# Kernel optimization log

Hardware: AMD Instinct MI355X
Metric: run time of the kernel (lower is better)

The kernel has to match this reference:

```python
import jax, jax.numpy as jnp
import numpy as np

N = 2048          # nodes
IN_DIM = 512      # in_dim
H = 8             # num_heads
HD = IN_DIM // H  # head_dim = 64
L = 5             # max_path_len
E = 32768         # edges
D_EDGE = 64       # edge_feat_dim


def setup_inputs() -> dict:
    key = jax.random.key(0)
    ks = jax.random.split(key, 14)
    w = 1.0 / np.sqrt(IN_DIM)
    return {
        "node_feat": jax.random.normal(ks[0], (N, IN_DIM), jnp.float32),
        "edge_index": jax.random.randint(ks[1], (2, E), 0, N, dtype=jnp.int32),
        "max_path_len": 5,
        "shortest_distances": jax.random.randint(ks[2], (N, N), 0, L + 1, dtype=jnp.int32),
        "shortest_paths": jax.random.randint(ks[3], (N, N, L), 0, E + 1, dtype=jnp.int32),  # E == padding row
        "edge_feat": jax.random.normal(ks[4], (E, D_EDGE), jnp.float32),
        "attention_mask": jnp.zeros((N, N), jnp.int32),
        "WQ": jax.random.normal(ks[5], (IN_DIM, IN_DIM), jnp.float32) * w,
        "bQ": jax.random.normal(ks[6], (IN_DIM,), jnp.float32) * 0.02,
        "WK": jax.random.normal(ks[7], (IN_DIM, IN_DIM), jnp.float32) * w,
        "bK": jax.random.normal(ks[8], (IN_DIM,), jnp.float32) * 0.02,
        "WV": jax.random.normal(ks[9], (IN_DIM, IN_DIM), jnp.float32) * w,
        "bV": jax.random.normal(ks[10], (IN_DIM,), jnp.float32) * 0.02,
        "WO": jax.random.normal(ks[11], (IN_DIM, IN_DIM), jnp.float32) * w,
        "bO": jnp.zeros((IN_DIM,), jnp.float32),
        "spatial_bias": jax.random.normal(ks[12], ((L + 1) * H, 1), jnp.float32) * 0.02,
        "edge_weight": jax.random.normal(ks[13], ((L + 1) * H, D_EDGE), jnp.float32) * 0.02,
    }


def reference(node_feat, edge_index, max_path_len, shortest_distances, shortest_paths,
              edge_feat, attention_mask, WQ, bQ, WK, bK, WV, bV, WO, bO,
              spatial_bias, edge_weight):
    Nn, D = node_feat.shape
    Lp = max_path_len  # min(max_path_len, max_shortest_path_len); distances reach Lp here

    Q = (node_feat @ WQ + bQ).reshape(Nn, H, HD)
    K = (node_feat @ WK + bK).reshape(Nn, H, HD)
    V = (node_feat @ WV + bV).reshape(Nn, H, HD)

    # QK^T / sqrt(head_dim), laid out [N, N, H] as in the original after permute
    scores = jnp.einsum('nhd,mhd->nmh', Q, K) / np.sqrt(HD).astype(np.float32)

    # SpatialEncoding: bias table [(L+1)*H, 1] -> [L+1, H]; gather by clamped distance
    sp_table = spatial_bias.reshape(Lp + 1, H)
    dist = jnp.clip(shortest_distances, 0, Lp)
    scores = scores + sp_table[dist]  # [N, N, H]

    # EdgeEncoding: einsum('xyld,ldh->xyh') refactored as per-edge projection then gather
    W_e = edge_weight[: Lp * H].reshape(Lp, H, D_EDGE)  # (reshape[L,H,D].permute -> [L,D,H])
    padded = jnp.concatenate([edge_feat, jnp.zeros((1, D_EDGE), edge_feat.dtype)], axis=0)
    T = jnp.einsum('ed,lhd->elh', padded, W_e)  # [E+1, L, H]
    sp = shortest_paths[:, :, :Lp]
    gathered = T[sp, jnp.arange(Lp)[None, None, :]]  # [N, N, L, H]
    scores = scores + gathered.sum(axis=2)

    mask = attention_mask.astype(bool)
    scores = jnp.where(mask[:, :, None], -jnp.inf, scores)

    # NOTE: original applies softmax over dim=-1 of the [N, N, H] tensor (the head axis);
    # faithfully reproduced here. Dropout is identity (eval / p for inference).
    attn = jax.nn.softmax(scores, axis=-1)

    out = jnp.einsum('nmh,mhd->nhd', attn, V).reshape(Nn, D)
    return out @ WO + bO
```

## Files before the change

kernel.cpp:

```cpp
#include <hip/hip_runtime.h>

#define NN     2048
#define DIM    512
#define NH     8
#define HD     64
#define NE     32768
#define EPAD   32832
#define CHUNKS 4
#define LOG2E  1.4426950408889634f

typedef __attribute__((ext_vector_type(8))) short bf16x8;
typedef __attribute__((ext_vector_type(4))) float f32x4;

#define MFMA(a,b,c) __builtin_amdgcn_mfma_f32_16x16x32_bf16((a),(b),(c),0,0,0)

__device__ __forceinline__ float bf2f(unsigned int u16){
  union { unsigned int i; float f; } v; v.i = u16 << 16; return v.f;
}
__device__ __forceinline__ unsigned short f2bf(float f){
  union { float ff; unsigned int i; } v; v.ff = f;
  return (unsigned short)((v.i + 0x7fffu + ((v.i >> 16) & 1u)) >> 16);
}

__global__ __launch_bounds__(256) void cvt_k(
    const float* __restrict__ X, const float* __restrict__ ef, const float* __restrict__ ew,
    unsigned short* __restrict__ Xb, unsigned short* __restrict__ pEF, unsigned short* __restrict__ pEW)
{
  long g = (long)blockIdx.x*256 + threadIdx.x;
  const long GX = (long)NN*DIM/8;
  const long GE = (long)EPAD*8;
  const float* src; unsigned short* dst; long off, lim8;
  if (g < GX){ src = X;  dst = Xb;  off = g;        lim8 = GX; }
  else if (g < GX+GE){ src = ef; dst = pEF; off = g-GX; lim8 = (long)NE*8; }
  else { off = g-GX-GE; if (off >= 512) return; src = ew; dst = pEW; lim8 = 320; }
  unsigned short o[8];
  if (off < lim8){
    #pragma unroll
    for (int i=0;i<8;i++) o[i] = f2bf(src[off*8+i]);
  } else {
    #pragma unroll
    for (int i=0;i<8;i++) o[i] = 0;
  }
  *(uint4*)(dst + off*8) = *(const uint4*)o;
}

__global__ __launch_bounds__(256) void transpose512(
    const float* __restrict__ a0, const float* __restrict__ a1,
    const float* __restrict__ a2, const float* __restrict__ a3,
    unsigned short* __restrict__ out)
{
  __shared__ unsigned short tile[32][33];
  const float* src = blockIdx.z==0 ? a0 : blockIdx.z==1 ? a1 : blockIdx.z==2 ? a2 : a3;
  unsigned short* dst = out + (size_t)blockIdx.z*DIM*DIM;
  int bx = blockIdx.x*32, by = blockIdx.y*32;
  int tx = threadIdx.x, ty = threadIdx.y;
  #pragma unroll
  for (int i=0;i<32;i+=8) tile[ty+i][tx] = f2bf(src[(size_t)(by+ty+i)*DIM + bx+tx]);
  __syncthreads();
  #pragma unroll
  for (int i=0;i<32;i+=8) dst[(size_t)(bx+ty+i)*DIM + by+tx] = tile[tx][ty+i];
}

__global__ __launch_bounds__(256) void gemm_bt(
    const unsigned short* __restrict__ A1, const unsigned short* __restrict__ A2,
    const float* __restrict__ bias, unsigned short* __restrict__ C, float* __restrict__ Cf,
    int M, int N, int K, int bias_row)
{
  int lane = threadIdx.x & 63, w = threadIdx.x >> 6;
  int quad = lane >> 4, low = lane & 15;
  int m0 = blockIdx.y*64 + w*16;
  int n0 = blockIdx.x*64;
  f32x4 acc[4];
  #pragma unroll
  for (int t=0;t<4;t++) acc[t] = (f32x4){0.f,0.f,0.f,0.f};
  for (int k0=0; k0<K; k0+=32){
    bf16x8 a = *(const bf16x8*)(A1 + (size_t)(m0+low)*K + k0 + quad*8);
    #pragma unroll
    for (int t=0;t<4;t++){
      bf16x8 b = *(const bf16x8*)(A2 + (size_t)(n0+16*t+low)*K + k0 + quad*8);
      acc[t] = MFMA(a, b, acc[t]);
    }
  }
  #pragma unroll
  for (int t=0;t<4;t++){
    #pragma unroll
    for (int r=0;r<4;r++){
      int row = m0 + quad*4 + r;
      int col = n0 + 16*t + low;
      float v = acc[t][r];
      if (bias) v += bias[bias_row ? row : col];
      if (Cf) Cf[(size_t)row*N + col] = v;
      else    C [(size_t)row*N + col] = f2bf(v);
    }
  }
}

__global__ __launch_bounds__(512) void attn_k(
    const unsigned short* __restrict__ Qb, const unsigned short* __restrict__ Kb,
    const unsigned short* __restrict__ Vt, const unsigned short* __restrict__ T2,
    const float* __restrict__ spb, const int* __restrict__ dist,
    const int* __restrict__ sp, const int* __restrict__ maskp,
    float* __restrict__ partO)
{
  __shared__ __attribute__((aligned(16))) float sld[NH][16][68];
  __shared__ float sptab[48];
  int tid = threadIdx.x;
  int lane = tid & 63, h = tid >> 6;
  int quad = lane >> 4, low = lane & 15;
  int q0 = blockIdx.x * 16;
  int chunk = blockIdx.y;
  if (tid < 48) sptab[tid] = spb[tid];

  bf16x8 aq[2];
  #pragma unroll
  for (int s=0;s<2;s++)
    aq[s] = *(const bf16x8*)(Qb + (size_t)(q0+low)*DIM + h*HD + s*32 + quad*8);

  f32x4 accO[4];
  #pragma unroll
  for (int t=0;t<4;t++) accO[t] = (f32x4){0.f,0.f,0.f,0.f};

  for (int jt=0; jt<8; ++jt){
    int m0 = chunk*512 + jt*64;
    __syncthreads();

    #pragma unroll
    for (int it=0; it<2; ++it){
      int p = tid + it*512;
      int qq = p >> 6, mm = p & 63;
      long pix = (long)(q0+qq)*NN + (m0+mm);
      int dd = dist[pix];
      dd = dd < 0 ? 0 : (dd > 5 ? 5 : dd);
      float b[8];
      #pragma unroll
      for (int x=0;x<8;x++) b[x] = sptab[dd*8 + x];
      #pragma unroll
      for (int l=0;l<5;l++){
        int e = sp[pix*5 + l];
        if ((unsigned)e > (unsigned)NE) e = NE;
        uint4 tv = *(const uint4*)(T2 + (size_t)e*64 + l*8);
        b[0] += bf2f(tv.x & 0xffffu); b[1] += bf2f(tv.x >> 16);
        b[2] += bf2f(tv.y & 0xffffu); b[3] += bf2f(tv.y >> 16);
        b[4] += bf2f(tv.z & 0xffffu); b[5] += bf2f(tv.z >> 16);
        b[6] += bf2f(tv.w & 0xffffu); b[7] += bf2f(tv.w >> 16);
      }
      int msk = maskp[pix];
      #pragma unroll
      for (int x=0;x<8;x++) sld[x][qq][mm] = msk ? -1e30f : b[x];
    }
    __syncthreads();

    f32x4 S[4];
    #pragma unroll
    for (int t=0;t<4;t++) S[t] = (f32x4){0.f,0.f,0.f,0.f};
    #pragma unroll
    for (int s=0;s<2;s++){
      #pragma unroll
      for (int t=0;t<4;t++){
        bf16x8 bk = *(const bf16x8*)(Kb + (size_t)(m0+16*t+low)*DIM + h*HD + s*32 + quad*8);
        S[t] = MFMA(aq[s], bk, S[t]);
      }
    }
    #pragma unroll
    for (int t=0;t<4;t++){
      #pragma unroll
      for (int r=0;r<4;r++){
        float* slot = &sld[h][quad*4+r][low+16*t];
        *slot = S[t][r]*0.125f + *slot;
      }
    }
    __syncthreads();

    #pragma unroll
    for (int it=0; it<2; ++it){
      int p = tid + it*512;
      int qq = p >> 6, mm = p & 63;
      float s0[8];
      #pragma unroll
      for (int x=0;x<8;x++) s0[x] = sld[x][qq][mm];
      float mx = s0[0];
      #pragma unroll
      for (int x=1;x<8;x++) mx = fmaxf(mx, s0[x]);
      float sum = 0.f;
      #pragma unroll
      for (int x=0;x<8;x++){ s0[x] = exp2f((s0[x]-mx)*LOG2E); sum += s0[x]; }
      float inv = (mx < -1e29f) ? 0.f : 1.f/sum;
      #pragma unroll
      for (int x=0;x<8;x++) sld[x][qq][mm] = s0[x]*inv;
    }
    __syncthreads();

    bf16x8 ap[2];
    #pragma unroll
    for (int s=0;s<2;s++){
      const float* pp = &sld[h][low][s*32 + quad*8];
      float4 x0 = *(const float4*)pp;
      float4 x1 = *(const float4*)(pp + 4);
      bf16x8 a;
      a[0]=(short)f2bf(x0.x); a[1]=(short)f2bf(x0.y); a[2]=(short)f2bf(x0.z); a[3]=(short)f2bf(x0.w);
      a[4]=(short)f2bf(x1.x); a[5]=(short)f2bf(x1.y); a[6]=(short)f2bf(x1.z); a[7]=(short)f2bf(x1.w);
      ap[s] = a;
    }
    #pragma unroll
    for (int s=0;s<2;s++){
      #pragma unroll
      for (int t=0;t<4;t++){
        bf16x8 bv = *(const bf16x8*)(Vt + (size_t)(h*HD + 16*t + low)*NN + m0 + s*32 + quad*8);
        accO[t] = MFMA(ap[s], bv, accO[t]);
      }
    }
  }

  #pragma unroll
  for (int t=0;t<4;t++){
    #pragma unroll
    for (int r=0;r<4;r++){
      int q = quad*4 + r;
      partO[(((size_t)chunk*NN + q0 + q)*NH + h)*HD + 16*t + low] = accO[t][r];
    }
  }
}

__global__ __launch_bounds__(512) void merge_k(const float* __restrict__ partO,
                                               unsigned short* __restrict__ Obf)
{
  size_t idx = (size_t)blockIdx.x*512 + threadIdx.x;
  float s = 0.f;
  #pragma unroll
  for (int c=0;c<CHUNKS;c++) s += partO[(size_t)c*NN*DIM + idx];
  Obf[idx] = f2bf(s);
}

extern "C" void kernel_launch(void* const* d_in, const int* in_sizes, int n_in,
                              void* d_out, int out_size, void* d_ws, size_t ws_size,
                              hipStream_t stream)
{
  const float* X    = (const float*)d_in[0];
  const int*  dist  = (const int*)d_in[3];
  const int*  sp    = (const int*)d_in[4];
  const float* ef   = (const float*)d_in[5];
  const int*  maskp = (const int*)d_in[6];
  const float* WQ   = (const float*)d_in[7];
  const float* bQ   = (const float*)d_in[8];
  const float* WK   = (const float*)d_in[9];
  const float* bK   = (const float*)d_in[10];
  const float* WV   = (const float*)d_in[11];
  const float* bV   = (const float*)d_in[12];
  const float* WO   = (const float*)d_in[13];
  const float* bO   = (const float*)d_in[14];
  const float* spb  = (const float*)d_in[15];
  const float* ew   = (const float*)d_in[16];

  char* ws = (char*)d_ws;
  unsigned short* Wt   = (unsigned short*)(ws + 0);
  unsigned short* Xb   = (unsigned short*)(ws + 2097152);
  unsigned short* Qb   = (unsigned short*)(ws + 4194304);
  unsigned short* Kb   = (unsigned short*)(ws + 6291456);
  unsigned short* Vtb  = (unsigned short*)(ws + 8388608);
  unsigned short* pEF  = (unsigned short*)(ws + 10485760);
  unsigned short* pEW  = (unsigned short*)(ws + 14688256);
  unsigned short* T2   = (unsigned short*)(ws + 14696448);
  unsigned short* Obf  = (unsigned short*)(ws + 18898944);
  float*          pO   = (float*)(ws + 20996096);

  cvt_k<<<dim3(1540), dim3(256), 0, stream>>>(X, ef, ew, Xb, pEF, pEW);
  transpose512<<<dim3(16,16,4), dim3(32,8), 0, stream>>>(WQ, WK, WV, WO, Wt);
  gemm_bt<<<dim3(1,513),  dim3(256), 0, stream>>>(pEF, pEW, (const float*)nullptr, T2, (float*)nullptr, EPAD, 64, 64, 0);
  gemm_bt<<<dim3(8,32),   dim3(256), 0, stream>>>(Xb,  Wt,          bQ, Qb,  (float*)nullptr, NN, DIM, DIM, 0);
  gemm_bt<<<dim3(8,32),   dim3(256), 0, stream>>>(Xb,  Wt + 262144, bK, Kb,  (float*)nullptr, NN, DIM, DIM, 0);
  gemm_bt<<<dim3(32,8),   dim3(256), 0, stream>>>(Wt + 524288, Xb,  bV, Vtb, (float*)nullptr, DIM, NN, DIM, 1);
  attn_k<<<dim3(128,CHUNKS), dim3(512), 0, stream>>>(Qb, Kb, Vtb, T2, spb, dist, sp, maskp, pO);
  merge_k<<<dim3(2048), dim3(512), 0, stream>>>(pO, Obf);
  gemm_bt<<<dim3(8,32),  dim3(256), 0, stream>>>(Obf, Wt + 786432, bO, (unsigned short*)nullptr, (float*)d_out, NN, DIM, DIM, 0);
}
```

Baseline: 430.1 us.

## Prefetch attention bias indices one tile ahead and raise parallelism

The attention kernel now loads the next tile's distance, mask and shortest-path edge indices into registers while the current tile is processed. This is meant to hide the latency of the dependent T2 gathers. The key range is split into 8 chunks instead of 4, which doubles the attention grid and the size of the partial-output buffer. The generic GEMM tile is narrowed from 64 to 32 columns, with its grids doubled to give more blocks. The costs are higher register pressure from the prefetched indices and more partial results for the merge step to combine.

```diff
diff --git a/kernel.cpp b/kernel.cpp
--- a/kernel.cpp
+++ b/kernel.cpp
@@ -6,7 +6,9 @@
 #define HD     64
 #define NE     32768
 #define EPAD   32832
-#define CHUNKS 4
+#define CHUNKS 8
+#define CHSZ   (NN/CHUNKS)
+#define NJT    (CHSZ/64)
 #define LOG2E  1.4426950408889634f
 
 typedef __attribute__((ext_vector_type(8))) short bf16x8;
@@ -69,20 +71,20 @@
   int lane = threadIdx.x & 63, w = threadIdx.x >> 6;
   int quad = lane >> 4, low = lane & 15;
   int m0 = blockIdx.y*64 + w*16;
-  int n0 = blockIdx.x*64;
-  f32x4 acc[4];
-  #pragma unroll
-  for (int t=0;t<4;t++) acc[t] = (f32x4){0.f,0.f,0.f,0.f};
+  int n0 = blockIdx.x*32;
+  f32x4 acc[2];
+  acc[0] = (f32x4){0.f,0.f,0.f,0.f};
+  acc[1] = (f32x4){0.f,0.f,0.f,0.f};
   for (int k0=0; k0<K; k0+=32){
     bf16x8 a = *(const bf16x8*)(A1 + (size_t)(m0+low)*K + k0 + quad*8);
     #pragma unroll
-    for (int t=0;t<4;t++){
+    for (int t=0;t<2;t++){
       bf16x8 b = *(const bf16x8*)(A2 + (size_t)(n0+16*t+low)*K + k0 + quad*8);
       acc[t] = MFMA(a, b, acc[t]);
     }
   }
   #pragma unroll
-  for (int t=0;t<4;t++){
+  for (int t=0;t<2;t++){
     #pragma unroll
     for (int r=0;r<4;r++){
       int row = m0 + quad*4 + r;
@@ -120,33 +122,62 @@
   #pragma unroll
   for (int t=0;t<4;t++) accO[t] = (f32x4){0.f,0.f,0.f,0.f};
 
-  for (int jt=0; jt<8; ++jt){
-    int m0 = chunk*512 + jt*64;
+  int pd[2], pm[2], pe[2][5];
+  #pragma unroll
+  for (int it=0; it<2; ++it){
+    int p = tid + it*512;
+    int qq = p >> 6, mm = p & 63;
+    long pix = (long)(q0+qq)*NN + (chunk*CHSZ + mm);
+    pd[it] = dist[pix]; pm[it] = maskp[pix];
+    #pragma unroll
+    for (int l=0;l<5;l++) pe[it][l] = sp[pix*5 + l];
+  }
+  __syncthreads();
+
+  for (int jt=0; jt<NJT; ++jt){
+    int m0 = chunk*CHSZ + jt*64;
+
+    float bb[2][8];
+    int mk[2];
+    #pragma unroll
+    for (int it=0; it<2; ++it){
+      mk[it] = pm[it];
+      int dd = pd[it];
+      dd = dd < 0 ? 0 : (dd > 5 ? 5 : dd);
+      #pragma unroll
+      for (int x=0;x<8;x++) bb[it][x] = sptab[dd*8 + x];
+      #pragma unroll
+      for (int l=0;l<5;l++){
+        int e = pe[it][l];
+        if ((unsigned)e > (unsigned)NE) e = NE;
+        uint4 tv = *(const uint4*)(T2 + (size_t)e*64 + l*8);
+        bb[it][0] += bf2f(tv.x & 0xffffu); bb[it][1] += bf2f(tv.x >> 16);
+        bb[it][2] += bf2f(tv.y & 0xffffu); bb[it][3] += bf2f(tv.y >> 16);
+        bb[it][4] += bf2f(tv.z & 0xffffu); bb[it][5] += bf2f(tv.z >> 16);
+        bb[it][6] += bf2f(tv.w & 0xffffu); bb[it][7] += bf2f(tv.w >> 16);
+      }
+    }
+
     __syncthreads();
 
     #pragma unroll
     for (int it=0; it<2; ++it){
       int p = tid + it*512;
       int qq = p >> 6, mm = p & 63;
-      long pix = (long)(q0+qq)*NN + (m0+mm);
-      int dd = dist[pix];
-      dd = dd < 0 ? 0 : (dd > 5 ? 5 : dd);
-      float b[8];
-      #pragma unroll
-      for (int x=0;x<8;x++) b[x] = sptab[dd*8 + x];
-      #pragma unroll
-      for (int l=0;l<5;l++){
-        int e = sp[pix*5 + l];
-        if ((unsigned)e > (unsigned)NE) e = NE;
-        uint4 tv = *(const uint4*)(T2 + (size_t)e*64 + l*8);
-        b[0] += bf2f(tv.x & 0xffffu); b[1] += bf2f(tv.x >> 16);
-        b[2] += bf2f(tv.y & 0xffffu); b[3] += bf2f(tv.y >> 16);
-        b[4] += bf2f(tv.z & 0xffffu); b[5] += bf2f(tv.z >> 16);
-        b[6] += bf2f(tv.w & 0xffffu); b[7] += bf2f(tv.w >> 16);
-      }
-      int msk = maskp[pix];
-      #pragma unroll
-      for (int x=0;x<8;x++) sld[x][qq][mm] = msk ? -1e30f : b[x];
+      #pragma unroll
+      for (int x=0;x<8;x++) sld[x][qq][mm] = mk[it] ? -1e30f : bb[it][x];
+    }
+
+    if (jt+1 < NJT){
+      #pragma unroll
+      for (int it=0; it<2; ++it){
+        int p = tid + it*512;
+        int qq = p >> 6, mm = p & 63;
+        long pix = (long)(q0+qq)*NN + (m0 + 64 + mm);
+        pd[it] = dist[pix]; pm[it] = maskp[pix];
+        #pragma unroll
+        for (int l=0;l<5;l++) pe[it][l] = sp[pix*5 + l];
+      }
     }
     __syncthreads();
 
@@ -265,11 +296,11 @@
 
   cvt_k<<<dim3(1540), dim3(256), 0, stream>>>(X, ef, ew, Xb, pEF, pEW);
   transpose512<<<dim3(16,16,4), dim3(32,8), 0, stream>>>(WQ, WK, WV, WO, Wt);
-  gemm_bt<<<dim3(1,513),  dim3(256), 0, stream>>>(pEF, pEW, (const float*)nullptr, T2, (float*)nullptr, EPAD, 64, 64, 0);
-  gemm_bt<<<dim3(8,32),   dim3(256), 0, stream>>>(Xb,  Wt,          bQ, Qb,  (float*)nullptr, NN, DIM, DIM, 0);
-  gemm_bt<<<dim3(8,32),   dim3(256), 0, stream>>>(Xb,  Wt + 262144, bK, Kb,  (float*)nullptr, NN, DIM, DIM, 0);
-  gemm_bt<<<dim3(32,8),   dim3(256), 0, stream>>>(Wt + 524288, Xb,  bV, Vtb, (float*)nullptr, DIM, NN, DIM, 1);
+  gemm_bt<<<dim3(2,513),  dim3(256), 0, stream>>>(pEF, pEW, (const float*)nullptr, T2, (float*)nullptr, EPAD, 64, 64, 0);
+  gemm_bt<<<dim3(16,32),  dim3(256), 0, stream>>>(Xb,  Wt,          bQ, Qb,  (float*)nullptr, NN, DIM, DIM, 0);
+  gemm_bt<<<dim3(16,32),  dim3(256), 0, stream>>>(Xb,  Wt + 262144, bK, Kb,  (float*)nullptr, NN, DIM, DIM, 0);
+  gemm_bt<<<dim3(64,8),   dim3(256), 0, stream>>>(Wt + 524288, Xb,  bV, Vtb, (float*)nullptr, DIM, NN, DIM, 1);
   attn_k<<<dim3(128,CHUNKS), dim3(512), 0, stream>>>(Qb, Kb, Vtb, T2, spb, dist, sp, maskp, pO);
   merge_k<<<dim3(2048), dim3(512), 0, stream>>>(pO, Obf);
-  gemm_bt<<<dim3(8,32),  dim3(256), 0, stream>>>(Obf, Wt + 786432, bO, (unsigned short*)nullptr, (float*)d_out, NN, DIM, DIM, 0);
-}
+  gemm_bt<<<dim3(16,32), dim3(256), 0, stream>>>(Obf, Wt + 786432, bO, (unsigned short*)nullptr, (float*)d_out, NN, DIM, DIM, 0);
+}
```

Result: faster. 411.0 us (-4.5%).
